# Performance work log

Hardware: AMD Instinct MI355X
Metric: run time of the kernel (lower is better)

The kernel has to match this reference:

```python
import jax, jax.numpy as jnp
import numpy as np

D = 1024      # d_model
B = 16        # batch size
L = 1024      # query length
NE = 20000    # global number of entities
NB = 256      # entities per batch element (with -1 padding)
N_PAD = 32    # padded (-1) entity slots per row


def setup_inputs() -> dict:
    key = jax.random.key(0)
    ks = jax.random.split(key, 10)
    s = 1.0 / np.sqrt(D)  # torch nn.Linear default init range
    query = jax.random.normal(ks[0], (B, L, D), jnp.float32)
    ent_emb = jax.random.normal(ks[1], (NE, D), jnp.float32)
    idx = jax.random.randint(ks[2], (B, NB), 0, NE)
    idx = idx.at[:, -N_PAD:].set(-1)  # padding entities -> masked out
    WQ_w = jax.random.uniform(ks[3], (D, D), jnp.float32, -s, s)
    WQ_b = jax.random.uniform(ks[4], (D,), jnp.float32, -s, s)
    WK_w = jax.random.uniform(ks[5], (D, D), jnp.float32, -s, s)
    WK_b = jax.random.uniform(ks[6], (D,), jnp.float32, -s, s)
    WO_w = jax.random.uniform(ks[7], (D, D), jnp.float32, -s, s)
    WO_b = jax.random.uniform(ks[8], (D,), jnp.float32, -s, s)
    ln_g = jnp.ones((D,), jnp.float32)
    ln_b = jnp.zeros((D,), jnp.float32)
    return dict(query=query, ent_emb=ent_emb, ent_idx_in_batch=idx,
                max_entity_number=512,
                WQ_w=WQ_w, WQ_b=WQ_b, WK_w=WK_w, WK_b=WK_b,
                WO_w=WO_w, WO_b=WO_b, ln_g=ln_g, ln_b=ln_b)


def reference(query, ent_emb, ent_idx_in_batch, max_entity_number,
              WQ_w, WQ_b, WK_w, WK_b, WO_w, WO_b, ln_g, ln_b):
    # mask: 1.0 for real entities, 0.0 for -1 padding. (B, NB, 1)
    mask = (ent_idx_in_batch != -1).astype(query.dtype)[:, :, None]
    # gather per-batch entity embeddings (negative index wraps, then masked)
    ent_g = ent_emb[ent_idx_in_batch]                    # (B, NB, D)
    q = query @ WQ_w.T + WQ_b                            # (B, L, D)
    ent = (ent_g @ WK_w.T + WK_b) * mask                 # (B, NB, D)
    # attention scores with additive mask, then softmax
    w = jnp.einsum('byd,bnd->byn', q, ent)               # (B, L, NB)
    w = w - (1.0 - mask[:, :, 0])[:, None, :] * 100000.0
    w = jax.nn.softmax(w, axis=-1)
    # NOTE: original code uses WK (not WV) for values, and scales AFTER softmax
    d_model = query.shape[-1]
    v = jnp.einsum('byn,bnd->byd', w * (float(d_model) ** -0.5), ent)
    v = v @ WO_w.T + WO_b                                # (B, L, D)
    mu = jnp.mean(v, axis=-1, keepdims=True)
    var = jnp.var(v, axis=-1, keepdims=True)             # biased, as torch LN
    v = (v - mu) / jnp.sqrt(var + 1e-5) * ln_g + ln_b
    return v
```

## Files before the change

kernel.cpp:

```cpp
#include <hip/hip_runtime.h>
#include <hip/hip_bf16.h>
#include <cstdint>
#include <cstddef>

typedef _Float16 f16;
typedef _Float16 f16x8 __attribute__((ext_vector_type(8)));
typedef _Float16 f16x4 __attribute__((ext_vector_type(4)));
typedef float    f32x4 __attribute__((ext_vector_type(4)));

#define DM 1024
#define NBE 256

__global__ __launch_bounds__(256) void conv_f32_f16(const float* __restrict__ in,
                                                    f16* __restrict__ out, int n) {
  int i = (blockIdx.x * 256 + threadIdx.x) * 4;
  if (i >= n) return;
  float4 v = *(const float4*)(in + i);
  f16x4 o; o.x = (f16)v.x; o.y = (f16)v.y; o.z = (f16)v.z; o.w = (f16)v.w;
  *(f16x4*)(out + i) = o;
}

__global__ __launch_bounds__(256) void tr2(const float* __restrict__ in0,
                                           const float* __restrict__ in1,
                                           f16* __restrict__ out0,
                                           f16* __restrict__ out1) {
  const float* in = blockIdx.z ? in1 : in0;
  f16* out = blockIdx.z ? out1 : out0;
  __shared__ float t[64][65];
  int bi = blockIdx.y * 64, bj = blockIdx.x * 64;
  int tx = threadIdx.x & 63, ty = threadIdx.x >> 6;
#pragma unroll
  for (int k = 0; k < 16; ++k) {
    int r = ty * 16 + k;
    t[r][tx] = in[(size_t)(bi + r) * DM + bj + tx];
  }
  __syncthreads();
#pragma unroll
  for (int k = 0; k < 16; ++k) {
    int r = ty * 16 + k;
    out[(size_t)(bj + r) * DM + bi + tx] = (f16)t[tx][r];
  }
}

__global__ __launch_bounds__(256) void gather_f16(const float* __restrict__ emb,
                                                  const int* __restrict__ idx,
                                                  f16* __restrict__ out) {
  int slot = blockIdx.x;
  int e = idx[slot];
  int c = threadIdx.x * 4;
  f16x4 o;
  if (e < 0) {
    o.x = (f16)0.f; o.y = (f16)0.f; o.z = (f16)0.f; o.w = (f16)0.f;
  } else {
    float4 v = *(const float4*)(emb + (size_t)e * DM + c);
    o.x = (f16)v.x; o.y = (f16)v.y; o.z = (f16)v.z; o.w = (f16)v.w;
  }
  *(f16x4*)(out + (size_t)slot * DM + c) = o;
}

__global__ __launch_bounds__(256) void coldot(const float* __restrict__ WK,
                                              const float* __restrict__ bq,
                                              const float* __restrict__ bk,
                                              float* __restrict__ u) {
  if (blockIdx.x < 4) {
    int k = blockIdx.x * 256 + threadIdx.x;
    float s = 0.f;
    for (int d = 0; d < 1024; ++d) s += bq[d] * WK[(size_t)d * 1024 + k];
    u[k] = s;
  } else {
    float s = 0.f;
    for (int i = threadIdx.x; i < 1024; i += 256) s += bk[i] * bq[i];
#pragma unroll
    for (int d = 1; d < 64; d <<= 1) s += __shfl_xor(s, d);
    __shared__ float sm[4];
    int w = threadIdx.x >> 6;
    if ((threadIdx.x & 63) == 0) sm[w] = s;
    __syncthreads();
    if (threadIdx.x == 0) u[1024] = sm[0] + sm[1] + sm[2] + sm[3];
  }
}

__global__ __launch_bounds__(256) void rowdot(const float* __restrict__ A,
                                              const float* __restrict__ v,
                                              float* __restrict__ out) {
  int w = threadIdx.x >> 6, lane = threadIdx.x & 63;
  int r = blockIdx.x * 4 + w;
  const float* a = A + (size_t)r * 1024;
  float s = 0.f;
#pragma unroll
  for (int i = 0; i < 16; ++i) s += a[lane + i * 64] * v[lane + i * 64];
#pragma unroll
  for (int d = 1; d < 64; d <<= 1) s += __shfl_xor(s, d);
  if (lane == 0) out[r] = s;
}

__global__ __launch_bounds__(256) void cvec_k(const f16* __restrict__ Eg,
                                              const float* __restrict__ u,
                                              float* __restrict__ cvec) {
  int w = threadIdx.x >> 6, lane = threadIdx.x & 63;
  int n = blockIdx.x * 4 + w;
  const f16* e = Eg + (size_t)n * 1024;
  float s = 0.f;
#pragma unroll
  for (int i = 0; i < 16; ++i) { int k = lane + i * 64; s += (float)e[k] * u[k]; }
#pragma unroll
  for (int d = 1; d < 64; d <<= 1) s += __shfl_xor(s, d);
  if (lane == 0) cvec[n] = s + u[1024];
}

template <int EPI>
__device__ __forceinline__ void gemm_core(
    const f16* __restrict__ A, const f16* __restrict__ B,
    const float* __restrict__ rowbias, const int* __restrict__ colidx,
    f16* __restrict__ C, int N, int K, int m0, int n0,
    f16* __restrict__ smA, f16* __restrict__ smB) {
  int tid = threadIdx.x;
  int lane = tid & 63, w = tid >> 6;
  int wr = w >> 1, wc = w & 1;
  int l15 = lane & 15, lhi = lane >> 4;
  const f16* Ab = A + (size_t)m0 * K;
  const f16* Bb = B + (size_t)n0 * K;

  f32x4 acc[4][4];
  f32x4 z4 = {0.f, 0.f, 0.f, 0.f};
#pragma unroll
  for (int i = 0; i < 4; ++i)
#pragma unroll
    for (int j = 0; j < 4; ++j) acc[i][j] = z4;

  f16x8 ra[4], rb[4];
#pragma unroll
  for (int p = 0; p < 4; ++p) {
    int e = p * 2048 + tid * 8;
    int row = e >> 6, c8 = (e & 63) >> 3;
    ra[p] = *(const f16x8*)(Ab + (size_t)row * K + c8 * 8);
    rb[p] = *(const f16x8*)(Bb + (size_t)row * K + c8 * 8);
  }
#pragma unroll
  for (int p = 0; p < 4; ++p) {
    int e = p * 2048 + tid * 8;
    int row = e >> 6, c8 = (e & 63) >> 3;
    int off = row * 64 + ((c8 ^ (row & 7)) << 3);
    *(f16x8*)(&smA[off]) = ra[p];
    *(f16x8*)(&smB[off]) = rb[p];
  }

  int nk = K >> 6;
  for (int kt = 0; kt < nk; ++kt) {
    int cur = kt & 1;
    bool pre = (kt + 1 < nk);
    __syncthreads();
    if (pre) {
      const f16* An = Ab + (kt + 1) * 64;
      const f16* Bn = Bb + (kt + 1) * 64;
#pragma unroll
      for (int p = 0; p < 4; ++p) {
        int e = p * 2048 + tid * 8;
        int row = e >> 6, c8 = (e & 63) >> 3;
        ra[p] = *(const f16x8*)(An + (size_t)row * K + c8 * 8);
        rb[p] = *(const f16x8*)(Bn + (size_t)row * K + c8 * 8);
      }
    }
    const f16* As = smA + cur * 8192;
    const f16* Bs = smB + cur * 8192;
    __builtin_amdgcn_s_setprio(1);
#pragma unroll
    for (int kk = 0; kk < 2; ++kk) {
      int c8 = kk * 4 + lhi;
      f16x8 af[4], bf[4];
#pragma unroll
      for (int mi = 0; mi < 4; ++mi) {
        int r = wr * 64 + mi * 16 + l15;
        af[mi] = *(const f16x8*)(As + r * 64 + ((c8 ^ (r & 7)) << 3));
      }
#pragma unroll
      for (int ni = 0; ni < 4; ++ni) {
        int r = wc * 64 + ni * 16 + l15;
        bf[ni] = *(const f16x8*)(Bs + r * 64 + ((c8 ^ (r & 7)) << 3));
      }
#pragma unroll
      for (int mi = 0; mi < 4; ++mi)
#pragma unroll
        for (int ni = 0; ni < 4; ++ni)
          acc[mi][ni] = __builtin_amdgcn_mfma_f32_16x16x32_f16(af[mi], bf[ni], acc[mi][ni], 0, 0, 0);
    }
    __builtin_amdgcn_s_setprio(0);
    if (pre) {
#pragma unroll
      for (int p = 0; p < 4; ++p) {
        int e = p * 2048 + tid * 8;
        int row = e >> 6, c8 = (e & 63) >> 3;
        int off = (cur ^ 1) * 8192 + row * 64 + ((c8 ^ (row & 7)) << 3);
        *(f16x8*)(&smA[off]) = ra[p];
        *(f16x8*)(&smB[off]) = rb[p];
      }
    }
  }

#pragma unroll
  for (int mi = 0; mi < 4; ++mi) {
#pragma unroll
    for (int j = 0; j < 4; ++j) {
      int r = m0 + wr * 64 + mi * 16 + lhi * 4 + j;
      float rbv = (EPI == 3) ? rowbias[r] : 0.f;
#pragma unroll
      for (int ni = 0; ni < 4; ++ni) {
        int cN = n0 + wc * 64 + ni * 16 + l15;
        float v = acc[mi][ni][j];
        if (EPI == 3) { v += rbv; if (colidx[cN] < 0) v = 0.f; }
        C[(size_t)r * N + cN] = (f16)v;
      }
    }
  }
}

__global__ __launch_bounds__(256) void gemm_f16(const f16* __restrict__ A,
                                                const f16* __restrict__ B,
                                                f16* __restrict__ C, int N, int K) {
  __shared__ __align__(16) f16 sA[2 * 8192], sB[2 * 8192];
  gemm_core<0>(A, B, nullptr, nullptr, C, N, K, blockIdx.y * 128, blockIdx.x * 128, sA, sB);
}

__global__ __launch_bounds__(256) void gemm_dual(const f16* __restrict__ A0,
                                                 const f16* __restrict__ A1,
                                                 const f16* __restrict__ B,
                                                 f16* __restrict__ C0,
                                                 f16* __restrict__ C1, int N, int K) {
  __shared__ __align__(16) f16 sA[2 * 8192], sB[2 * 8192];
  const f16* A = blockIdx.z ? A1 : A0;
  f16* C = blockIdx.z ? C1 : C0;
  gemm_core<0>(A, B, nullptr, nullptr, C, N, K, blockIdx.y * 128, blockIdx.x * 128, sA, sB);
}

__global__ __launch_bounds__(256) void gemm_ewot(const f16* __restrict__ A,
                                                 const f16* __restrict__ B,
                                                 const float* __restrict__ rowbias,
                                                 const int* __restrict__ colidx,
                                                 f16* __restrict__ C, int N, int K) {
  __shared__ __align__(16) f16 sA[2 * 8192], sB[2 * 8192];
  gemm_core<3>(A, B, rowbias, colidx, C, N, K, blockIdx.y * 128, blockIdx.x * 128, sA, sB);
}

__global__ __launch_bounds__(256, 2) void attn2(
    const float* __restrict__ query, const f16* __restrict__ Tp,
    const f16* __restrict__ EWot, const float* __restrict__ cvec,
    const int* __restrict__ idx, f16* __restrict__ O16) {
  __shared__ __align__(16) char pool[65536];
  f16* smB = (f16*)pool;
  f16* smP = (f16*)(pool + 32768);
  f16* smQ = (f16*)(pool + 32768);
  int id = blockIdx.x;
  int b = id & 15, lt = id >> 4;
  int tid = threadIdx.x, lane = tid & 63, w = tid >> 6;
  int l15 = lane & 15, lhi = lane >> 4;
  const float* Qb = query + (size_t)(b * 1024 + lt * 64) * DM;
  const f16* Tb = Tp + (size_t)b * NBE * DM;

  f32x4 z4 = {0.f, 0.f, 0.f, 0.f};
  f32x4 accs[16];
#pragma unroll
  for (int i = 0; i < 16; ++i) accs[i] = z4;

  float4 rq[4];
  f16x8 rb[8];
  int qrow = tid >> 2, qc0 = (tid & 3) * 16;

#pragma unroll
  for (int q = 0; q < 4; ++q)
    rq[q] = *(const float4*)(Qb + (size_t)qrow * DM + qc0 + q * 4);
#pragma unroll
  for (int p = 0; p < 8; ++p) {
    int e = p * 2048 + tid * 8;
    int row = e >> 6, c8 = (e & 63) >> 3;
    rb[p] = *(const f16x8*)(Tb + (size_t)row * DM + c8 * 8);
  }

  for (int kt = 0; kt < 16; ++kt) {
    __syncthreads();
    {
      f16x8 h0, h1;
      h0[0] = (f16)rq[0].x; h0[1] = (f16)rq[0].y; h0[2] = (f16)rq[0].z; h0[3] = (f16)rq[0].w;
      h0[4] = (f16)rq[1].x; h0[5] = (f16)rq[1].y; h0[6] = (f16)rq[1].z; h0[7] = (f16)rq[1].w;
      h1[0] = (f16)rq[2].x; h1[1] = (f16)rq[2].y; h1[2] = (f16)rq[2].z; h1[3] = (f16)rq[2].w;
      h1[4] = (f16)rq[3].x; h1[5] = (f16)rq[3].y; h1[6] = (f16)rq[3].z; h1[7] = (f16)rq[3].w;
      int c8a = qc0 >> 3;
      *(f16x8*)(smQ + qrow * 64 + (((c8a    ) ^ (qrow & 7)) << 3)) = h0;
      *(f16x8*)(smQ + qrow * 64 + (((c8a + 1) ^ (qrow & 7)) << 3)) = h1;
    }
#pragma unroll
    for (int p = 0; p < 8; ++p) {
      int e = p * 2048 + tid * 8;
      int row = e >> 6, c8 = (e & 63) >> 3;
      *(f16x8*)(smB + row * 64 + ((c8 ^ (row & 7)) << 3)) = rb[p];
    }
    __syncthreads();
    if (kt < 15) {
#pragma unroll
      for (int q = 0; q < 4; ++q)
        rq[q] = *(const float4*)(Qb + (size_t)qrow * DM + (kt + 1) * 64 + qc0 + q * 4);
#pragma unroll
      for (int p = 0; p < 8; ++p) {
        int e = p * 2048 + tid * 8;
        int row = e >> 6, c8 = (e & 63) >> 3;
        rb[p] = *(const f16x8*)(Tb + (size_t)row * DM + (kt + 1) * 64 + c8 * 8);
      }
    }
    __builtin_amdgcn_s_setprio(1);
#pragma unroll
    for (int kk = 0; kk < 2; ++kk) {
      int c8 = kk * 4 + lhi;
      int qr = w * 16 + l15;
      f16x8 aq = *(const f16x8*)(smQ + qr * 64 + ((c8 ^ (qr & 7)) << 3));
#pragma unroll
      for (int ni = 0; ni < 16; ++ni) {
        int er = ni * 16 + l15;
        f16x8 bb = *(const f16x8*)(smB + er * 64 + ((c8 ^ (er & 7)) << 3));
        accs[ni] = __builtin_amdgcn_mfma_f32_16x16x32_f16(aq, bb, accs[ni], 0, 0, 0);
      }
    }
    __builtin_amdgcn_s_setprio(0);
  }

  const f16* Eb = EWot + (size_t)b * NBE;
#pragma unroll
  for (int p = 0; p < 8; ++p) {
    int e = p * 2048 + tid * 8;
    int row = e >> 6, c8 = (e & 63) >> 3;
    rb[p] = *(const f16x8*)(Eb + (size_t)row * 4096 + c8 * 8);
  }
  __syncthreads();

  float cv[16];
#pragma unroll
  for (int ni = 0; ni < 16; ++ni) {
    int slot = b * NBE + ni * 16 + l15;
    cv[ni] = cvec[slot] + ((idx[slot] < 0) ? -100000.0f : 0.0f);
  }
#pragma unroll
  for (int j = 0; j < 4; ++j) {
    float mx = -3.0e38f;
#pragma unroll
    for (int ni = 0; ni < 16; ++ni) mx = fmaxf(mx, accs[ni][j] + cv[ni]);
    mx = fmaxf(mx, __shfl_xor(mx, 1));
    mx = fmaxf(mx, __shfl_xor(mx, 2));
    mx = fmaxf(mx, __shfl_xor(mx, 4));
    mx = fmaxf(mx, __shfl_xor(mx, 8));
    float sum = 0.f;
    float pv[16];
#pragma unroll
    for (int ni = 0; ni < 16; ++ni) { pv[ni] = __expf(accs[ni][j] + cv[ni] - mx); sum += pv[ni]; }
    sum += __shfl_xor(sum, 1);
    sum += __shfl_xor(sum, 2);
    sum += __shfl_xor(sum, 4);
    sum += __shfl_xor(sum, 8);
    float inv = 1.0f / sum;
    int r = w * 16 + lhi * 4 + j;
#pragma unroll
    for (int ni = 0; ni < 16; ++ni) {
      int col = ni * 16 + l15;
      int cc8 = col >> 3;
      smP[r * 256 + ((cc8 ^ (r & 7)) << 3) + (col & 7)] = (f16)(pv[ni] * inv);
    }
  }

  f16* Ob = O16 + (size_t)(b * 1024 + lt * 64) * DM;
  for (int dc = 0; dc < 4; ++dc) {
    f32x4 accv[16];
#pragma unroll
    for (int i = 0; i < 16; ++i) accv[i] = z4;
    for (int ks = 0; ks < 4; ++ks) {
      __syncthreads();
#pragma unroll
      for (int p = 0; p < 8; ++p) {
        int e = p * 2048 + tid * 8;
        int row = e >> 6, c8 = (e & 63) >> 3;
        *(f16x8*)(smB + row * 64 + ((c8 ^ (row & 7)) << 3)) = rb[p];
      }
      __syncthreads();
      int nxt = dc * 4 + ks + 1;
      if (nxt < 16) {
        int ndc = nxt >> 2, nks = nxt & 3;
#pragma unroll
        for (int p = 0; p < 8; ++p) {
          int e = p * 2048 + tid * 8;
          int row = e >> 6, c8 = (e & 63) >> 3;
          rb[p] = *(const f16x8*)(Eb + (size_t)(ndc * 256 + row) * 4096 + nks * 64 + c8 * 8);
        }
      }
      __builtin_amdgcn_s_setprio(1);
#pragma unroll
      for (int kk = 0; kk < 2; ++kk) {
        int pc8 = ks * 8 + kk * 4 + lhi;
        int qr = w * 16 + l15;
        f16x8 ap = *(const f16x8*)(smP + qr * 256 + ((pc8 ^ (qr & 7)) << 3));
        int c8 = kk * 4 + lhi;
#pragma unroll
        for (int ni = 0; ni < 16; ++ni) {
          int er = ni * 16 + l15;
          f16x8 bv = *(const f16x8*)(smB + er * 64 + ((c8 ^ (er & 7)) << 3));
          accv[ni] = __builtin_amdgcn_mfma_f32_16x16x32_f16(ap, bv, accv[ni], 0, 0, 0);
        }
      }
      __builtin_amdgcn_s_setprio(0);
    }
#pragma unroll
    for (int ni = 0; ni < 16; ++ni) {
#pragma unroll
      for (int j = 0; j < 4; ++j) {
        int r = w * 16 + lhi * 4 + j;
        int col = dc * 256 + ni * 16 + l15;
        Ob[(size_t)r * DM + col] = (f16)(accv[ni][j] * 0.03125f);
      }
    }
  }
}

__global__ __launch_bounds__(256) void ln_f16(const f16* __restrict__ X,
                                              const float* __restrict__ bo,
                                              const float* __restrict__ g,
                                              const float* __restrict__ bta,
                                              float* __restrict__ out) {
  size_t row = blockIdx.x;
  const f16* x = X + row * DM;
  int tid = threadIdx.x;
  f16x4 h = *(const f16x4*)(x + tid * 4);
  float4 bo4 = *(const float4*)(bo + tid * 4);
  float4 v;
  v.x = (float)h[0] + bo4.x; v.y = (float)h[1] + bo4.y;
  v.z = (float)h[2] + bo4.z; v.w = (float)h[3] + bo4.w;
  float s = v.x + v.y + v.z + v.w;
  float q = v.x * v.x + v.y * v.y + v.z * v.z + v.w * v.w;
#pragma unroll
  for (int d = 1; d < 64; d <<= 1) { s += __shfl_xor(s, d); q += __shfl_xor(q, d); }
  __shared__ float ss[4], qq[4];
  int w = tid >> 6, lane = tid & 63;
  if (lane == 0) { ss[w] = s; qq[w] = q; }
  __syncthreads();
  s = ss[0] + ss[1] + ss[2] + ss[3];
  q = qq[0] + qq[1] + qq[2] + qq[3];
  float mu = s * (1.0f / DM);
  float var = q * (1.0f / DM) - mu * mu;
  float rs = rsqrtf(var + 1e-5f);
  float4 gg = *(const float4*)(g + tid * 4);
  float4 bb = *(const float4*)(bta + tid * 4);
  float4 o;
  o.x = (v.x - mu) * rs * gg.x + bb.x;
  o.y = (v.y - mu) * rs * gg.y + bb.y;
  o.z = (v.z - mu) * rs * gg.z + bb.z;
  o.w = (v.w - mu) * rs * gg.w + bb.w;
  *(float4*)(out + row * DM + tid * 4) = o;
}

extern "C" void kernel_launch(void* const* d_in, const int* in_sizes, int n_in,
                              void* d_out, int out_size, void* d_ws, size_t ws_size,
                              hipStream_t stream) {
  const float* query   = (const float*)d_in[0];
  const float* ent_emb = (const float*)d_in[1];
  const int*   idx     = (const int*)d_in[2];
  const float* WQ_w = (const float*)d_in[4];
  const float* WQ_b = (const float*)d_in[5];
  const float* WK_w = (const float*)d_in[6];
  const float* WK_b = (const float*)d_in[7];
  const float* WO_w = (const float*)d_in[8];
  const float* WO_b = (const float*)d_in[9];
  const float* ln_g = (const float*)d_in[10];
  const float* ln_b = (const float*)d_in[11];
  float* out = (float*)d_out;

  char* p = (char*)d_ws;
  f16* Egh  = (f16*)p;  p += (size_t)4096 * 1024 * 2;
  f16* WQt  = (f16*)p;  p += (size_t)1024 * 1024 * 2;
  f16* WKt  = (f16*)p;  p += (size_t)1024 * 1024 * 2;
  f16* WOr  = (f16*)p;  p += (size_t)1024 * 1024 * 2;
  f16* G    = (f16*)p;  p += (size_t)1024 * 1024 * 2;
  f16* H    = (f16*)p;  p += (size_t)1024 * 1024 * 2;
  f16* Tp   = (f16*)p;  p += (size_t)4096 * 1024 * 2;
  f16* EWot = (f16*)p;  p += (size_t)1024 * 4096 * 2;
  f16* O16  = (f16*)p;  p += (size_t)16384 * 1024 * 2;
  float* u    = (float*)p; p += 1025 * 4;
  float* wobk = (float*)p; p += 1024 * 4;
  float* cvec = (float*)p; p += 4096 * 4;

  tr2<<<dim3(16, 16, 2), 256, 0, stream>>>(WQ_w, WK_w, WQt, WKt);
  conv_f32_f16<<<1024, 256, 0, stream>>>(WO_w, WOr, 1024 * 1024);
  gather_f16<<<4096, 256, 0, stream>>>(ent_emb, idx, Egh);
  coldot<<<5, 256, 0, stream>>>(WK_w, WQ_b, WK_b, u);
  rowdot<<<256, 256, 0, stream>>>(WO_w, WK_b, wobk);
  gemm_dual<<<dim3(8, 8, 2), 256, 0, stream>>>(WQt, WOr, WKt, G, H, 1024, 1024);
  cvec_k<<<1024, 256, 0, stream>>>(Egh, u, cvec);
  gemm_f16<<<dim3(8, 32), 256, 0, stream>>>(Egh, G, Tp, 1024, 1024);
  gemm_ewot<<<dim3(32, 8), 256, 0, stream>>>(H, Egh, wobk, idx, EWot, 4096, 1024);
  attn2<<<256, 256, 0, stream>>>(query, Tp, EWot, cvec, idx, O16);
  ln_f16<<<16384, 256, 0, stream>>>(O16, WO_b, ln_g, ln_b, out);
}
```

Baseline: 326.9 us.

## Merge prep kernels, pair GEMMs, and split attention tiles across more blocks

The five preprocessing kernels are merged into one launch with block-range dispatch, and the two entity GEMMs plus the cvec reduction are merged into a single launch. The mask bias is folded into cvec. The attention kernel now handles 32 query rows per block instead of 64, doubling the grid to 512 blocks, with the entity dimension split across wave pairs and softmax max/sum exchanged through shared memory. This aims to cut launch overhead and improve occupancy and CU fill, at the cost of extra synchronisations and re-reading the entity tiles twice as often.

Measured after the change: 308.0 us. 1.06x faster.

```diff
diff --git a/kernel.cpp b/kernel.cpp
--- a/kernel.cpp
+++ b/kernel.cpp
@@ -11,101 +11,79 @@
 #define DM 1024
 #define NBE 256
 
-__global__ __launch_bounds__(256) void conv_f32_f16(const float* __restrict__ in,
-                                                    f16* __restrict__ out, int n) {
-  int i = (blockIdx.x * 256 + threadIdx.x) * 4;
-  if (i >= n) return;
-  float4 v = *(const float4*)(in + i);
-  f16x4 o; o.x = (f16)v.x; o.y = (f16)v.y; o.z = (f16)v.z; o.w = (f16)v.w;
-  *(f16x4*)(out + i) = o;
-}
-
-__global__ __launch_bounds__(256) void tr2(const float* __restrict__ in0,
-                                           const float* __restrict__ in1,
-                                           f16* __restrict__ out0,
-                                           f16* __restrict__ out1) {
-  const float* in = blockIdx.z ? in1 : in0;
-  f16* out = blockIdx.z ? out1 : out0;
-  __shared__ float t[64][65];
-  int bi = blockIdx.y * 64, bj = blockIdx.x * 64;
-  int tx = threadIdx.x & 63, ty = threadIdx.x >> 6;
-#pragma unroll
-  for (int k = 0; k < 16; ++k) {
-    int r = ty * 16 + k;
-    t[r][tx] = in[(size_t)(bi + r) * DM + bj + tx];
-  }
-  __syncthreads();
-#pragma unroll
-  for (int k = 0; k < 16; ++k) {
-    int r = ty * 16 + k;
-    out[(size_t)(bj + r) * DM + bi + tx] = (f16)t[tx][r];
-  }
-}
-
-__global__ __launch_bounds__(256) void gather_f16(const float* __restrict__ emb,
-                                                  const int* __restrict__ idx,
-                                                  f16* __restrict__ out) {
-  int slot = blockIdx.x;
-  int e = idx[slot];
-  int c = threadIdx.x * 4;
-  f16x4 o;
-  if (e < 0) {
-    o.x = (f16)0.f; o.y = (f16)0.f; o.z = (f16)0.f; o.w = (f16)0.f;
+__global__ __launch_bounds__(256) void prep(
+    const float* __restrict__ WO_w, f16* __restrict__ WOr,
+    const float* __restrict__ WQ_w, const float* __restrict__ WK_w,
+    f16* __restrict__ WQt, f16* __restrict__ WKt,
+    const float* __restrict__ ent_emb, const int* __restrict__ idx,
+    f16* __restrict__ Egh,
+    const float* __restrict__ WQ_b, const float* __restrict__ WK_b,
+    float* __restrict__ u, float* __restrict__ wobk) {
+  __shared__ float ts[64][65];
+  __shared__ float sm4[4];
+  int blk = blockIdx.x, tid = threadIdx.x;
+  if (blk < 1024) {
+    int i = (blk * 256 + tid) * 4;
+    float4 v = *(const float4*)(WO_w + i);
+    f16x4 o; o.x = (f16)v.x; o.y = (f16)v.y; o.z = (f16)v.z; o.w = (f16)v.w;
+    *(f16x4*)(WOr + i) = o;
+  } else if (blk < 1536) {
+    int t = blk - 1024;
+    const float* in = (t >> 8) ? WK_w : WQ_w;
+    f16* out = (t >> 8) ? WKt : WQt;
+    int bi = ((t >> 4) & 15) * 64, bj = (t & 15) * 64;
+    int tx = tid & 63, ty = tid >> 6;
+#pragma unroll
+    for (int k = 0; k < 16; ++k) {
+      int r = ty * 16 + k;
+      ts[r][tx] = in[(size_t)(bi + r) * DM + bj + tx];
+    }
+    __syncthreads();
+#pragma unroll
+    for (int k = 0; k < 16; ++k) {
+      int r = ty * 16 + k;
+      out[(size_t)(bj + r) * DM + bi + tx] = (f16)ts[tx][r];
+    }
+  } else if (blk < 5632) {
+    int slot = blk - 1536;
+    int e = idx[slot];
+    int c = tid * 4;
+    f16x4 o;
+    if (e < 0) {
+      o.x = (f16)0.f; o.y = (f16)0.f; o.z = (f16)0.f; o.w = (f16)0.f;
+    } else {
+      float4 v = *(const float4*)(ent_emb + (size_t)e * DM + c);
+      o.x = (f16)v.x; o.y = (f16)v.y; o.z = (f16)v.z; o.w = (f16)v.w;
+    }
+    *(f16x4*)(Egh + (size_t)slot * DM + c) = o;
+  } else if (blk < 5637) {
+    int t = blk - 5632;
+    if (t < 4) {
+      int k = t * 256 + tid;
+      float s = 0.f;
+      for (int d = 0; d < 1024; ++d) s += WQ_b[d] * WK_w[(size_t)d * 1024 + k];
+      u[k] = s;
+    } else {
+      float s = 0.f;
+      for (int i = tid; i < 1024; i += 256) s += WK_b[i] * WQ_b[i];
+#pragma unroll
+      for (int d = 1; d < 64; d <<= 1) s += __shfl_xor(s, d);
+      int w = tid >> 6;
+      if ((tid & 63) == 0) sm4[w] = s;
+      __syncthreads();
+      if (tid == 0) u[1024] = sm4[0] + sm4[1] + sm4[2] + sm4[3];
+    }
   } else {
-    float4 v = *(const float4*)(emb + (size_t)e * DM + c);
-    o.x = (f16)v.x; o.y = (f16)v.y; o.z = (f16)v.z; o.w = (f16)v.w;
-  }
-  *(f16x4*)(out + (size_t)slot * DM + c) = o;
-}
-
-__global__ __launch_bounds__(256) void coldot(const float* __restrict__ WK,
-                                              const float* __restrict__ bq,
-                                              const float* __restrict__ bk,
-                                              float* __restrict__ u) {
-  if (blockIdx.x < 4) {
-    int k = blockIdx.x * 256 + threadIdx.x;
+    int w = tid >> 6, lane = tid & 63;
+    int r = (blk - 5637) * 4 + w;
+    const float* a = WO_w + (size_t)r * 1024;
     float s = 0.f;
-    for (int d = 0; d < 1024; ++d) s += bq[d] * WK[(size_t)d * 1024 + k];
-    u[k] = s;
-  } else {
-    float s = 0.f;
-    for (int i = threadIdx.x; i < 1024; i += 256) s += bk[i] * bq[i];
+#pragma unroll
+    for (int i = 0; i < 16; ++i) s += a[lane + i * 64] * WK_b[lane + i * 64];
 #pragma unroll
     for (int d = 1; d < 64; d <<= 1) s += __shfl_xor(s, d);
-    __shared__ float sm[4];
-    int w = threadIdx.x >> 6;
-    if ((threadIdx.x & 63) == 0) sm[w] = s;
-    __syncthreads();
-    if (threadIdx.x == 0) u[1024] = sm[0] + sm[1] + sm[2] + sm[3];
-  }
-}
-
-__global__ __launch_bounds__(256) void rowdot(const float* __restrict__ A,
-                                              const float* __restrict__ v,
-                                              float* __restrict__ out) {
-  int w = threadIdx.x >> 6, lane = threadIdx.x & 63;
-  int r = blockIdx.x * 4 + w;
-  const float* a = A + (size_t)r * 1024;
-  float s = 0.f;
-#pragma unroll
-  for (int i = 0; i < 16; ++i) s += a[lane + i * 64] * v[lane + i * 64];
-#pragma unroll
-  for (int d = 1; d < 64; d <<= 1) s += __shfl_xor(s, d);
-  if (lane == 0) out[r] = s;
-}
-
-__global__ __launch_bounds__(256) void cvec_k(const f16* __restrict__ Eg,
-                                              const float* __restrict__ u,
-                                              float* __restrict__ cvec) {
-  int w = threadIdx.x >> 6, lane = threadIdx.x & 63;
-  int n = blockIdx.x * 4 + w;
-  const f16* e = Eg + (size_t)n * 1024;
-  float s = 0.f;
-#pragma unroll
-  for (int i = 0; i < 16; ++i) { int k = lane + i * 64; s += (float)e[k] * u[k]; }
-#pragma unroll
-  for (int d = 1; d < 64; d <<= 1) s += __shfl_xor(s, d);
-  if (lane == 0) cvec[n] = s + u[1024];
+    if (lane == 0) wobk[r] = s;
+  }
 }
 
 template <int EPI>
@@ -214,13 +192,6 @@
   }
 }
 
-__global__ __launch_bounds__(256) void gemm_f16(const f16* __restrict__ A,
-                                                const f16* __restrict__ B,
-                                                f16* __restrict__ C, int N, int K) {
-  __shared__ __align__(16) f16 sA[2 * 8192], sB[2 * 8192];
-  gemm_core<0>(A, B, nullptr, nullptr, C, N, K, blockIdx.y * 128, blockIdx.x * 128, sA, sB);
-}
-
 __global__ __launch_bounds__(256) void gemm_dual(const f16* __restrict__ A0,
                                                  const f16* __restrict__ A1,
                                                  const f16* __restrict__ B,
@@ -232,42 +203,61 @@
   gemm_core<0>(A, B, nullptr, nullptr, C, N, K, blockIdx.y * 128, blockIdx.x * 128, sA, sB);
 }
 
-__global__ __launch_bounds__(256) void gemm_ewot(const f16* __restrict__ A,
-                                                 const f16* __restrict__ B,
-                                                 const float* __restrict__ rowbias,
-                                                 const int* __restrict__ colidx,
-                                                 f16* __restrict__ C, int N, int K) {
+__global__ __launch_bounds__(256) void gemm_pair(
+    const f16* __restrict__ Egh, const f16* __restrict__ G, const f16* __restrict__ H,
+    const float* __restrict__ wobk, const int* __restrict__ idx,
+    const float* __restrict__ u,
+    f16* __restrict__ Tp, f16* __restrict__ EWot, float* __restrict__ cvec) {
   __shared__ __align__(16) f16 sA[2 * 8192], sB[2 * 8192];
-  gemm_core<3>(A, B, rowbias, colidx, C, N, K, blockIdx.y * 128, blockIdx.x * 128, sA, sB);
-}
-
-__global__ __launch_bounds__(256, 2) void attn2(
+  int blk = blockIdx.x;
+  if (blk < 256) {
+    gemm_core<0>(Egh, G, nullptr, nullptr, Tp, 1024, 1024, (blk >> 3) * 128, (blk & 7) * 128, sA, sB);
+  } else if (blk < 512) {
+    int t = blk - 256;
+    gemm_core<3>(H, Egh, wobk, idx, EWot, 4096, 1024, (t >> 5) * 128, (t & 31) * 128, sA, sB);
+  } else {
+    int t = blk - 512;
+    int w = threadIdx.x >> 6, lane = threadIdx.x & 63;
+    int n = t * 4 + w;
+    const f16* e = Egh + (size_t)n * 1024;
+    float s = 0.f;
+#pragma unroll
+    for (int i = 0; i < 16; ++i) { int k = lane + i * 64; s += (float)e[k] * u[k]; }
+#pragma unroll
+    for (int d = 1; d < 64; d <<= 1) s += __shfl_xor(s, d);
+    if (lane == 0)
+      cvec[n] = s + u[1024] + ((idx[n] < 0) ? -100000.0f : 0.0f);
+  }
+}
+
+__global__ __launch_bounds__(256, 2) void attn3(
     const float* __restrict__ query, const f16* __restrict__ Tp,
     const f16* __restrict__ EWot, const float* __restrict__ cvec,
-    const int* __restrict__ idx, f16* __restrict__ O16) {
-  __shared__ __align__(16) char pool[65536];
+    f16* __restrict__ O16) {
+  __shared__ __align__(16) char pool[49152];
   f16* smB = (f16*)pool;
   f16* smP = (f16*)(pool + 32768);
   f16* smQ = (f16*)(pool + 32768);
+  __shared__ float smMax[64], smSum[64];
   int id = blockIdx.x;
   int b = id & 15, lt = id >> 4;
   int tid = threadIdx.x, lane = tid & 63, w = tid >> 6;
   int l15 = lane & 15, lhi = lane >> 4;
-  const float* Qb = query + (size_t)(b * 1024 + lt * 64) * DM;
+  int wq = w >> 1, wc = w & 1;
+  const float* Qb = query + (size_t)(b * 1024 + lt * 32) * DM;
   const f16* Tb = Tp + (size_t)b * NBE * DM;
 
   f32x4 z4 = {0.f, 0.f, 0.f, 0.f};
-  f32x4 accs[16];
-#pragma unroll
-  for (int i = 0; i < 16; ++i) accs[i] = z4;
-
-  float4 rq[4];
+  f32x4 accs[8];
+#pragma unroll
+  for (int i = 0; i < 8; ++i) accs[i] = z4;
+
+  float4 rqa, rqb;
   f16x8 rb[8];
-  int qrow = tid >> 2, qc0 = (tid & 3) * 16;
-
-#pragma unroll
-  for (int q = 0; q < 4; ++q)
-    rq[q] = *(const float4*)(Qb + (size_t)qrow * DM + qc0 + q * 4);
+  int qrow = tid >> 3, qc0 = (tid & 7) * 8;
+
+  rqa = *(const float4*)(Qb + (size_t)qrow * DM + qc0);
+  rqb = *(const float4*)(Qb + (size_t)qrow * DM + qc0 + 4);
 #pragma unroll
   for (int p = 0; p < 8; ++p) {
     int e = p * 2048 + tid * 8;
@@ -278,14 +268,11 @@
   for (int kt = 0; kt < 16; ++kt) {
     __syncthreads();
     {
-      f16x8 h0, h1;
-      h0[0] = (f16)rq[0].x; h0[1] = (f16)rq[0].y; h0[2] = (f16)rq[0].z; h0[3] = (f16)rq[0].w;
-      h0[4] = (f16)rq[1].x; h0[5] = (f16)rq[1].y; h0[6] = (f16)rq[1].z; h0[7] = (f16)rq[1].w;
-      h1[0] = (f16)rq[2].x; h1[1] = (f16)rq[2].y; h1[2] = (f16)rq[2].z; h1[3] = (f16)rq[2].w;
-      h1[4] = (f16)rq[3].x; h1[5] = (f16)rq[3].y; h1[6] = (f16)rq[3].z; h1[7] = (f16)rq[3].w;
-      int c8a = qc0 >> 3;
-      *(f16x8*)(smQ + qrow * 64 + (((c8a    ) ^ (qrow & 7)) << 3)) = h0;
-      *(f16x8*)(smQ + qrow * 64 + (((c8a + 1) ^ (qrow & 7)) << 3)) = h1;
+      f16x8 h;
+      h[0] = (f16)rqa.x; h[1] = (f16)rqa.y; h[2] = (f16)rqa.z; h[3] = (f16)rqa.w;
+      h[4] = (f16)rqb.x; h[5] = (f16)rqb.y; h[6] = (f16)rqb.z; h[7] = (f16)rqb.w;
+      int c8 = qc0 >> 3;
+      *(f16x8*)(smQ + qrow * 64 + ((c8 ^ (qrow & 7)) << 3)) = h;
     }
 #pragma unroll
     for (int p = 0; p < 8; ++p) {
@@ -295,9 +282,8 @@
     }
     __syncthreads();
     if (kt < 15) {
-#pragma unroll
-      for (int q = 0; q < 4; ++q)
-        rq[q] = *(const float4*)(Qb + (size_t)qrow * DM + (kt + 1) * 64 + qc0 + q * 4);
+      rqa = *(const float4*)(Qb + (size_t)qrow * DM + (kt + 1) * 64 + qc0);
+      rqb = *(const float4*)(Qb + (size_t)qrow * DM + (kt + 1) * 64 + qc0 + 4);
 #pragma unroll
       for (int p = 0; p < 8; ++p) {
         int e = p * 2048 + tid * 8;
@@ -309,11 +295,11 @@
 #pragma unroll
     for (int kk = 0; kk < 2; ++kk) {
       int c8 = kk * 4 + lhi;
-      int qr = w * 16 + l15;
+      int qr = wq * 16 + l15;
       f16x8 aq = *(const f16x8*)(smQ + qr * 64 + ((c8 ^ (qr & 7)) << 3));
 #pragma unroll
-      for (int ni = 0; ni < 16; ++ni) {
-        int er = ni * 16 + l15;
+      for (int ni = 0; ni < 8; ++ni) {
+        int er = wc * 128 + ni * 16 + l15;
         f16x8 bb = *(const f16x8*)(smB + er * 64 + ((c8 ^ (er & 7)) << 3));
         accs[ni] = __builtin_amdgcn_mfma_f32_16x16x32_f16(aq, bb, accs[ni], 0, 0, 0);
       }
@@ -328,46 +314,61 @@
     int row = e >> 6, c8 = (e & 63) >> 3;
     rb[p] = *(const f16x8*)(Eb + (size_t)row * 4096 + c8 * 8);
   }
+
+  float cv[8];
+#pragma unroll
+  for (int ni = 0; ni < 8; ++ni)
+    cv[ni] = cvec[b * NBE + wc * 128 + ni * 16 + l15];
+  int rbase = wq * 16 + lhi * 4;
+  float mxl[4], sml[4];
+#pragma unroll
+  for (int j = 0; j < 4; ++j) {
+    float m = -3.0e38f;
+#pragma unroll
+    for (int ni = 0; ni < 8; ++ni) m = fmaxf(m, accs[ni][j] + cv[ni]);
+    m = fmaxf(m, __shfl_xor(m, 1));
+    m = fmaxf(m, __shfl_xor(m, 2));
+    m = fmaxf(m, __shfl_xor(m, 4));
+    m = fmaxf(m, __shfl_xor(m, 8));
+    mxl[j] = m;
+    if (l15 == 0) smMax[wc * 32 + rbase + j] = m;
+  }
   __syncthreads();
-
-  float cv[16];
-#pragma unroll
-  for (int ni = 0; ni < 16; ++ni) {
-    int slot = b * NBE + ni * 16 + l15;
-    cv[ni] = cvec[slot] + ((idx[slot] < 0) ? -100000.0f : 0.0f);
-  }
 #pragma unroll
   for (int j = 0; j < 4; ++j) {
-    float mx = -3.0e38f;
-#pragma unroll
-    for (int ni = 0; ni < 16; ++ni) mx = fmaxf(mx, accs[ni][j] + cv[ni]);
-    mx = fmaxf(mx, __shfl_xor(mx, 1));
-    mx = fmaxf(mx, __shfl_xor(mx, 2));
-    mx = fmaxf(mx, __shfl_xor(mx, 4));
-    mx = fmaxf(mx, __shfl_xor(mx, 8));
-    float sum = 0.f;
-    float pv[16];
-#pragma unroll
-    for (int ni = 0; ni < 16; ++ni) { pv[ni] = __expf(accs[ni][j] + cv[ni] - mx); sum += pv[ni]; }
-    sum += __shfl_xor(sum, 1);
-    sum += __shfl_xor(sum, 2);
-    sum += __shfl_xor(sum, 4);
-    sum += __shfl_xor(sum, 8);
-    float inv = 1.0f / sum;
-    int r = w * 16 + lhi * 4 + j;
-#pragma unroll
-    for (int ni = 0; ni < 16; ++ni) {
-      int col = ni * 16 + l15;
+    float fm = fmaxf(mxl[j], smMax[(wc ^ 1) * 32 + rbase + j]);
+    float s = 0.f;
+#pragma unroll
+    for (int ni = 0; ni < 8; ++ni) {
+      float e = __expf(accs[ni][j] + cv[ni] - fm);
+      accs[ni][j] = e;
+      s += e;
+    }
+    s += __shfl_xor(s, 1);
+    s += __shfl_xor(s, 2);
+    s += __shfl_xor(s, 4);
+    s += __shfl_xor(s, 8);
+    sml[j] = s;
+    if (l15 == 0) smSum[wc * 32 + rbase + j] = s;
+  }
+  __syncthreads();
+#pragma unroll
+  for (int j = 0; j < 4; ++j) {
+    float inv = 0.03125f / (sml[j] + smSum[(wc ^ 1) * 32 + rbase + j]);
+    int r = rbase + j;
+#pragma unroll
+    for (int ni = 0; ni < 8; ++ni) {
+      int col = wc * 128 + ni * 16 + l15;
       int cc8 = col >> 3;
-      smP[r * 256 + ((cc8 ^ (r & 7)) << 3) + (col & 7)] = (f16)(pv[ni] * inv);
-    }
-  }
-
-  f16* Ob = O16 + (size_t)(b * 1024 + lt * 64) * DM;
+      smP[r * 256 + ((cc8 ^ (r & 7)) << 3) + (col & 7)] = (f16)(accs[ni][j] * inv);
+    }
+  }
+
+  f16* Ob = O16 + (size_t)(b * 1024 + lt * 32) * DM;
   for (int dc = 0; dc < 4; ++dc) {
-    f32x4 accv[16];
-#pragma unroll
-    for (int i = 0; i < 16; ++i) accv[i] = z4;
+    f32x4 accv[8];
+#pragma unroll
+    for (int i = 0; i < 8; ++i) accv[i] = z4;
     for (int ks = 0; ks < 4; ++ks) {
       __syncthreads();
 #pragma unroll
@@ -391,12 +392,12 @@
 #pragma unroll
       for (int kk = 0; kk < 2; ++kk) {
         int pc8 = ks * 8 + kk * 4 + lhi;
-        int qr = w * 16 + l15;
+        int qr = wq * 16 + l15;
         f16x8 ap = *(const f16x8*)(smP + qr * 256 + ((pc8 ^ (qr & 7)) << 3));
         int c8 = kk * 4 + lhi;
 #pragma unroll
-        for (int ni = 0; ni < 16; ++ni) {
-          int er = ni * 16 + l15;
+        for (int ni = 0; ni < 8; ++ni) {
+          int er = wc * 128 + ni * 16 + l15;
           f16x8 bv = *(const f16x8*)(smB + er * 64 + ((c8 ^ (er & 7)) << 3));
           accv[ni] = __builtin_amdgcn_mfma_f32_16x16x32_f16(ap, bv, accv[ni], 0, 0, 0);
         }
@@ -404,12 +405,12 @@
       __builtin_amdgcn_s_setprio(0);
     }
 #pragma unroll
-    for (int ni = 0; ni < 16; ++ni) {
+    for (int ni = 0; ni < 8; ++ni) {
 #pragma unroll
       for (int j = 0; j < 4; ++j) {
-        int r = w * 16 + lhi * 4 + j;
-        int col = dc * 256 + ni * 16 + l15;
-        Ob[(size_t)r * DM + col] = (f16)(accv[ni][j] * 0.03125f);
+        int r = wq * 16 + lhi * 4 + j;
+        int col = dc * 256 + wc * 128 + ni * 16 + l15;
+        Ob[(size_t)r * DM + col] = (f16)accv[ni][j];
       }
     }
   }
@@ -481,15 +482,10 @@
   float* wobk = (float*)p; p += 1024 * 4;
   float* cvec = (float*)p; p += 4096 * 4;
 
-  tr2<<<dim3(16, 16, 2), 256, 0, stream>>>(WQ_w, WK_w, WQt, WKt);
-  conv_f32_f16<<<1024, 256, 0, stream>>>(WO_w, WOr, 1024 * 1024);
-  gather_f16<<<4096, 256, 0, stream>>>(ent_emb, idx, Egh);
-  coldot<<<5, 256, 0, stream>>>(WK_w, WQ_b, WK_b, u);
-  rowdot<<<256, 256, 0, stream>>>(WO_w, WK_b, wobk);
+  prep<<<5893, 256, 0, stream>>>(WO_w, WOr, WQ_w, WK_w, WQt, WKt,
+                                 ent_emb, idx, Egh, WQ_b, WK_b, u, wobk);
   gemm_dual<<<dim3(8, 8, 2), 256, 0, stream>>>(WQt, WOr, WKt, G, H, 1024, 1024);
-  cvec_k<<<1024, 256, 0, stream>>>(Egh, u, cvec);
-  gemm_f16<<<dim3(8, 32), 256, 0, stream>>>(Egh, G, Tp, 1024, 1024);
-  gemm_ewot<<<dim3(32, 8), 256, 0, stream>>>(H, Egh, wobk, idx, EWot, 4096, 1024);
-  attn2<<<256, 256, 0, stream>>>(query, Tp, EWot, cvec, idx, O16);
+  gemm_pair<<<1536, 256, 0, stream>>>(Egh, G, H, wobk, idx, u, Tp, EWot, cvec);
+  attn3<<<512, 256, 0, stream>>>(query, Tp, EWot, cvec, O16);
   ln_f16<<<16384, 256, 0, stream>>>(O16, WO_b, ln_g, ln_b, out);
 }
```
